# Kernel optimization log

Hardware: AMD Instinct MI355X
Metric: run time of the kernel (lower is better)

Reference implementation:

```python
import jax, jax.numpy as jnp
import numpy as np

N_NODES = 100000
N_EDGES = 640000
DIM = 128
N_LAYERS = 3


def setup_inputs() -> dict:
    key = jax.random.key(0)
    k1, k2, k3, k4, k5 = jax.random.split(key, 5)
    nodes = jax.random.normal(k1, (N_NODES, DIM), dtype=jnp.float32)
    edges = jax.random.randint(k2, (2, N_EDGES), 0, N_NODES, dtype=jnp.int64)
    # GCNConv weights: one [DIM, DIM] linear + bias per layer
    W = jax.random.normal(k3, (N_LAYERS, DIM, DIM), dtype=jnp.float32) * (1.0 / np.sqrt(DIM))
    b = jnp.zeros((N_LAYERS, DIM), dtype=jnp.float32)
    # classifier head Linear(DIM, 2)
    clf_W = jax.random.normal(k4, (DIM, 2), dtype=jnp.float32) * (1.0 / np.sqrt(DIM))
    clf_b = jnp.zeros((2,), dtype=jnp.float32)
    return {"nodes": nodes, "edges": edges, "W": W, "b": b, "clf_W": clf_W, "clf_b": clf_b}


def _gcn_layer(x, src, dst, dinv, W, b):
    # PyG GCNConv: x' = D^{-1/2} (A + I) D^{-1/2} (x W) + b
    x = x @ W                                      # [N, D]
    norm = dinv[src] * dinv[dst]                   # [E+N]
    msgs = x[src] * norm[:, None]                  # gather + scale, [E+N, D]
    return jax.ops.segment_sum(msgs, dst, num_segments=x.shape[0]) + b


def reference(nodes, edges, W, b, clf_W, clf_b):
    N = nodes.shape[0]
    loops = jnp.arange(N, dtype=edges.dtype)
    src = jnp.concatenate([edges[0], loops])       # add self-loops
    dst = jnp.concatenate([edges[1], loops])
    deg = jax.ops.segment_sum(jnp.ones_like(dst, dtype=nodes.dtype), dst, num_segments=N)
    dinv = jnp.where(deg > 0, jax.lax.rsqrt(deg), 0.0)
    x = nodes
    for i in range(W.shape[0]):
        x = jax.nn.relu(_gcn_layer(x, src, dst, dinv, W[i], b[i]))
    return x @ clf_W + clf_b                       # [N, 2]
```

## Files before the change

kernel.cpp:

```cpp
#include <hip/hip_runtime.h>
#include <hip/hip_bf16.h>

#define N_NODES 100000
#define N_EDGES 640000
#define DIM 128
#define NE_TOT (N_NODES + N_EDGES)

typedef unsigned short u16;
typedef unsigned int u32;
typedef __attribute__((ext_vector_type(8))) short bf16x8;
typedef __attribute__((ext_vector_type(4))) float f32x4;
typedef __attribute__((ext_vector_type(8))) unsigned short us8;

__device__ __forceinline__ u16 f2bf(float f) {
    u32 u = __float_as_uint(f);
    u32 r = (u + 0x7fffu + ((u >> 16) & 1u)) >> 16;
    return (u16)r;
}
__device__ __forceinline__ float bf2f(u16 h) { return __uint_as_float(((u32)h) << 16); }

__device__ __forceinline__ void gload16(const void* g, void* l) {
    __builtin_amdgcn_global_load_lds(
        (const __attribute__((address_space(1))) u32*)g,
        (__attribute__((address_space(3))) u32*)l, 16, 0, 0);
}


__global__ void init_deg_kernel(int* deg, int n) {
    int i = blockIdx.x * blockDim.x + threadIdx.x;
    if (i < n) deg[i] = 1;
}

__global__ void count_deg_kernel(const int* __restrict__ edges, int* deg, int e) {
    int i = blockIdx.x * blockDim.x + threadIdx.x;
    if (i < e) atomicAdd(&deg[edges[N_EDGES + i]], 1);
}

__global__ void scan1_kernel(const int* __restrict__ deg, int* off, int* bsums, int n) {
    __shared__ int lds[256];
    int t = threadIdx.x;
    int base = blockIdx.x * 1024 + t * 4;
    int v[4]; int s = 0;
#pragma unroll
    for (int j = 0; j < 4; j++) { int idx = base + j; v[j] = (idx < n) ? deg[idx] : 0; s += v[j]; }
    lds[t] = s; __syncthreads();
    for (int d = 1; d < 256; d <<= 1) {
        int x = 0;
        if (t >= d) x = lds[t - d];
        __syncthreads();
        if (t >= d) lds[t] += x;
        __syncthreads();
    }
    if (t == 255) bsums[blockIdx.x] = lds[255];
    int run = lds[t] - s;
#pragma unroll
    for (int j = 0; j < 4; j++) { int idx = base + j; if (idx < n) off[idx] = run; run += v[j]; }
}

__global__ void scan2_kernel(int* bsums, int nchunks) {
    __shared__ int lds[128];
    int t = threadIdx.x;
    int v = (t < nchunks) ? bsums[t] : 0;
    lds[t] = v; __syncthreads();
    for (int d = 1; d < 128; d <<= 1) {
        int x = 0;
        if (t >= d) x = lds[t - d];
        __syncthreads();
        if (t >= d) lds[t] += x;
        __syncthreads();
    }
    if (t < nchunks) bsums[t] = lds[t] - v;
}

__global__ void scan3_kernel(int* off, const int* __restrict__ bsums, const int* __restrict__ deg,
                             int* cursor, float* dinv, int n) {
    int i = blockIdx.x * blockDim.x + threadIdx.x;
    if (i < n) {
        int o = off[i] + bsums[i >> 10];
        off[i] = o;
        cursor[i] = o;
        dinv[i] = 1.0f / sqrtf((float)deg[i]);
    }
}

__global__ void fill_csr_kernel(const int* __restrict__ edges, int* cursor, int* csr) {
    int i = blockIdx.x * blockDim.x + threadIdx.x;
    if (i < N_NODES) {
        int p = atomicAdd(&cursor[i], 1);
        csr[p] = i;
    } else if (i < NE_TOT) {
        int e = i - N_NODES;
        int s = edges[e];
        int d = edges[N_EDGES + e];
        int p = atomicAdd(&cursor[d], 1);
        csr[p] = s;
    }
}

__global__ void wsplit_kernel(const float* __restrict__ W, u16* __restrict__ WhiT, u16* __restrict__ WloT) {
    int i = blockIdx.x * 256 + threadIdx.x;
    int l = i >> 14; int r = i & 16383; int k = r >> 7; int c = r & 127;
    float w = W[i];
    u16 h = f2bf(w);
    u16 lo = f2bf(w - bf2f(h));
    u32 inner = ((u32)(k * 2)) ^ (((u32)c & 7u) << 4);
    size_t db = (size_t)l * 32768 + (size_t)c * 256 + inner;
    *(u16*)((char*)WhiT + db) = h;
    *(u16*)((char*)WloT + db) = lo;
}

__global__ void aggregate_kernel(const float* __restrict__ x, u16* __restrict__ yhi, u16* __restrict__ ylo,
                                 const int* __restrict__ off, const int* __restrict__ csr,
                                 const float* __restrict__ dinv, int n) {
    int wid = (blockIdx.x * blockDim.x + threadIdx.x) >> 6;
    int lane = threadIdx.x & 63;
    if (wid >= n) return;
    int start = off[wid];
    int end = (wid == n - 1) ? NE_TOT : off[wid + 1];
    int d0 = lane * 2;
    float ax = 0.f, ay = 0.f;
    for (int k = start; k < end; k++) {
        int s = csr[k];
        float w = dinv[s];
        float2 xv = *reinterpret_cast<const float2*>(x + (size_t)s * DIM + d0);
        ax += xv.x * w;
        ay += xv.y * w;
    }
    float di = dinv[wid];
    float vx = ax * di, vy = ay * di;
    u16 hx = f2bf(vx); u16 lx = f2bf(vx - bf2f(hx));
    u16 hy = f2bf(vy); u16 ly = f2bf(vy - bf2f(hy));
    u32 inner = ((u32)(lane * 4)) ^ (((u32)wid & 7u) << 4);
    *(u32*)((char*)yhi + (size_t)wid * 256 + inner) = (u32)hx | ((u32)hy << 16);
    *(u32*)((char*)ylo + (size_t)wid * 256 + inner) = (u32)lx | ((u32)ly << 16);
}

__device__ __forceinline__ bf16x8 lds_frag(const char* base, int row, int kbyte) {
    int off = row * 256 + (kbyte ^ ((row & 7) << 4));
    return __builtin_bit_cast(bf16x8, *(const us8*)(base + off));
}

__global__ __launch_bounds__(512, 1) void gemm_mfma_kernel(
        const u16* __restrict__ Yhi, const u16* __restrict__ Ylo,
        const u16* __restrict__ WhiT, const u16* __restrict__ WloT,
        const float* __restrict__ bias, float* __restrict__ out, int M) {
    __shared__ char smem[131072];
    char* Ah = smem;
    char* Al = smem + 32768;
    char* Bh = smem + 65536;
    char* Bl = smem + 98304;
    const int t = threadIdx.x;
    const int lane = t & 63, w = t >> 6;
    const int rowbase = blockIdx.x * 128;

#pragma unroll
    for (int it = 0; it < 4; it++) {
        int p = w * 4096 + it * 1024 + lane * 16;
        int rl = p >> 8;
        int rg = rowbase + rl; rg = (rg < M) ? rg : (M - 1);
        int inner = p & 255;
        gload16((const char*)Yhi + (size_t)rg * 256 + inner, Ah + w * 4096 + it * 1024);
        gload16((const char*)Ylo + (size_t)rg * 256 + inner, Al + w * 4096 + it * 1024);
        gload16((const char*)WhiT + p, Bh + w * 4096 + it * 1024);
        gload16((const char*)WloT + p, Bl + w * 4096 + it * 1024);
    }
    __syncthreads();

    const int wr = w >> 1, wc = w & 1;
    const int lr = lane & 15, kh = lane >> 4;
    f32x4 acc[2][4] = {};

#pragma unroll
    for (int ks = 0; ks < 4; ks++) {
        int kb = ks * 64 + kh * 16;
        bf16x8 ah[2], al[2], bh[4], bl[4];
#pragma unroll
        for (int ri = 0; ri < 2; ri++) {
            ah[ri] = lds_frag(Ah, wr * 32 + ri * 16 + lr, kb);
            al[ri] = lds_frag(Al, wr * 32 + ri * 16 + lr, kb);
        }
#pragma unroll
        for (int ci = 0; ci < 4; ci++) {
            bh[ci] = lds_frag(Bh, wc * 64 + ci * 16 + lr, kb);
            bl[ci] = lds_frag(Bl, wc * 64 + ci * 16 + lr, kb);
        }
#pragma unroll
        for (int ri = 0; ri < 2; ri++)
#pragma unroll
            for (int ci = 0; ci < 4; ci++) {
                acc[ri][ci] = __builtin_amdgcn_mfma_f32_16x16x32_bf16(ah[ri], bh[ci], acc[ri][ci], 0, 0, 0);
                acc[ri][ci] = __builtin_amdgcn_mfma_f32_16x16x32_bf16(ah[ri], bl[ci], acc[ri][ci], 0, 0, 0);
                acc[ri][ci] = __builtin_amdgcn_mfma_f32_16x16x32_bf16(al[ri], bh[ci], acc[ri][ci], 0, 0, 0);
            }
    }

#pragma unroll
    for (int ri = 0; ri < 2; ri++)
#pragma unroll
        for (int ci = 0; ci < 4; ci++) {
            int col = wc * 64 + ci * 16 + lr;
            float bc = bias[col];
            int r0 = rowbase + wr * 32 + ri * 16 + kh * 4;
#pragma unroll
            for (int j = 0; j < 4; j++) {
                int r = r0 + j;
                if (r < M) out[(size_t)r * 128 + col] = fmaxf(acc[ri][ci][j] + bc, 0.f);
            }
        }
}

__global__ void classifier_kernel(const float* __restrict__ x, const float* __restrict__ clfW,
                                  const float* __restrict__ clfb, float* __restrict__ out, int n) {
    int wid = (blockIdx.x * blockDim.x + threadIdx.x) >> 6;
    int lane = threadIdx.x & 63;
    if (wid >= n) return;
    float w00 = clfW[2 * lane], w01 = clfW[2 * lane + 1];
    float w10 = clfW[2 * (lane + 64)], w11 = clfW[2 * (lane + 64) + 1];
    float x0 = x[(size_t)wid * DIM + lane];
    float x1 = x[(size_t)wid * DIM + lane + 64];
    float a0 = x0 * w00 + x1 * w10;
    float a1 = x0 * w01 + x1 * w11;
#pragma unroll
    for (int d = 32; d > 0; d >>= 1) {
        a0 += __shfl_down(a0, d);
        a1 += __shfl_down(a1, d);
    }
    if (lane == 0) {
        out[2 * wid]     = a0 + clfb[0];
        out[2 * wid + 1] = a1 + clfb[1];
    }
}

extern "C" void kernel_launch(void* const* d_in, const int* in_sizes, int n_in,
                              void* d_out, int out_size, void* d_ws, size_t ws_size,
                              hipStream_t stream) {
    const float* nodes = (const float*)d_in[0];
    const int*   edges = (const int*)d_in[1];
    const float* W     = (const float*)d_in[2];
    const float* b     = (const float*)d_in[3];
    const float* clfW  = (const float*)d_in[4];
    const float* clfb  = (const float*)d_in[5];
    float* out = (float*)d_out;

    const int N = N_NODES, E = N_EDGES;

    float* X    = (float*)d_ws;
    u16* Yhi    = (u16*)(X + (size_t)N * DIM);
    u16* Ylo    = Yhi + (size_t)N * DIM;
    u16* WhiT   = Ylo + (size_t)N * DIM;
    u16* WloT   = WhiT + 3 * DIM * DIM;
    float* dinv = (float*)(WloT + 3 * DIM * DIM);
    int* deg    = (int*)(dinv + N);
    int* off    = deg + N;
    int* cursor = off + N;
    int* csr    = cursor + N;
    int* bsums  = csr + NE_TOT;

    const int nchunks = (N + 1023) / 1024;

    wsplit_kernel<<<(3 * DIM * DIM) / 256, 256, 0, stream>>>(W, WhiT, WloT);
    init_deg_kernel<<<(N + 255) / 256, 256, 0, stream>>>(deg, N);
    count_deg_kernel<<<(E + 255) / 256, 256, 0, stream>>>(edges, deg, E);
    scan1_kernel<<<nchunks, 256, 0, stream>>>(deg, off, bsums, N);
    scan2_kernel<<<1, 128, 0, stream>>>(bsums, nchunks);
    scan3_kernel<<<(N + 255) / 256, 256, 0, stream>>>(off, bsums, deg, cursor, dinv, N);
    fill_csr_kernel<<<(NE_TOT + 255) / 256, 256, 0, stream>>>(edges, cursor, csr);

    const int aggBlocks = (N + 3) / 4;
    const int gemmBlocks = (N + 127) / 128;

    aggregate_kernel<<<aggBlocks, 256, 0, stream>>>(nodes, Yhi, Ylo, off, csr, dinv, N);
    gemm_mfma_kernel<<<gemmBlocks, 512, 0, stream>>>(Yhi, Ylo, WhiT, WloT, b, X, N);

    aggregate_kernel<<<aggBlocks, 256, 0, stream>>>(X, Yhi, Ylo, off, csr, dinv, N);
    gemm_mfma_kernel<<<gemmBlocks, 512, 0, stream>>>(Yhi, Ylo, WhiT + DIM * DIM, WloT + DIM * DIM,
                                                     b + DIM, X, N);

    aggregate_kernel<<<aggBlocks, 256, 0, stream>>>(X, Yhi, Ylo, off, csr, dinv, N);
    gemm_mfma_kernel<<<gemmBlocks, 512, 0, stream>>>(Yhi, Ylo, WhiT + 2 * DIM * DIM, WloT + 2 * DIM * DIM,
                                                     b + 2 * DIM, X, N);

    classifier_kernel<<<aggBlocks, 256, 0, stream>>>(X, clfW, clfb, out, N);
}
```

Baseline: 558.4 us.

## Aggregate four nodes per wavefront and read GEMM weights from global memory

The aggregation kernel now assigns 16 lanes per node (4 nodes per wave). Each lane loads two float4 vectors per edge and writes 16-byte bf16 hi/lo chunks, which raises memory-level parallelism and vector width for the gather. The GEMM drops the LDS staging of the split weights and reads weight fragments straight from global memory through lds_frag. This halves LDS use and allows more blocks per CU. It risks uncoalesced global weight reads in the inner MFMA loop, and lds_frag applied to a global pointer relies on generic addressing.

```diff
diff --git a/kernel.cpp b/kernel.cpp
--- a/kernel.cpp
+++ b/kernel.cpp
@@ -112,27 +112,40 @@
 __global__ void aggregate_kernel(const float* __restrict__ x, u16* __restrict__ yhi, u16* __restrict__ ylo,
                                  const int* __restrict__ off, const int* __restrict__ csr,
                                  const float* __restrict__ dinv, int n) {
-    int wid = (blockIdx.x * blockDim.x + threadIdx.x) >> 6;
+    int gw = (blockIdx.x * blockDim.x + threadIdx.x) >> 6;
     int lane = threadIdx.x & 63;
-    if (wid >= n) return;
-    int start = off[wid];
-    int end = (wid == n - 1) ? NE_TOT : off[wid + 1];
-    int d0 = lane * 2;
-    float ax = 0.f, ay = 0.f;
+    int grp = lane >> 4;
+    int l4  = lane & 15;
+    int node = gw * 4 + grp;
+    if (node >= n) return;
+    int start = off[node];
+    int end = (node == n - 1) ? NE_TOT : off[node + 1];
+    float a[8] = {0.f, 0.f, 0.f, 0.f, 0.f, 0.f, 0.f, 0.f};
     for (int k = start; k < end; k++) {
         int s = csr[k];
         float w = dinv[s];
-        float2 xv = *reinterpret_cast<const float2*>(x + (size_t)s * DIM + d0);
-        ax += xv.x * w;
-        ay += xv.y * w;
-    }
-    float di = dinv[wid];
-    float vx = ax * di, vy = ay * di;
-    u16 hx = f2bf(vx); u16 lx = f2bf(vx - bf2f(hx));
-    u16 hy = f2bf(vy); u16 ly = f2bf(vy - bf2f(hy));
-    u32 inner = ((u32)(lane * 4)) ^ (((u32)wid & 7u) << 4);
-    *(u32*)((char*)yhi + (size_t)wid * 256 + inner) = (u32)hx | ((u32)hy << 16);
-    *(u32*)((char*)ylo + (size_t)wid * 256 + inner) = (u32)lx | ((u32)ly << 16);
+        const float* row = x + (size_t)s * DIM + l4 * 8;
+        float4 v0 = *reinterpret_cast<const float4*>(row);
+        float4 v1 = *reinterpret_cast<const float4*>(row + 4);
+        a[0] += v0.x * w; a[1] += v0.y * w; a[2] += v0.z * w; a[3] += v0.w * w;
+        a[4] += v1.x * w; a[5] += v1.y * w; a[6] += v1.z * w; a[7] += v1.w * w;
+    }
+    float di = dinv[node];
+    u16 h[8], lo[8];
+#pragma unroll
+    for (int j = 0; j < 8; j++) {
+        float v = a[j] * di;
+        h[j]  = f2bf(v);
+        lo[j] = f2bf(v - bf2f(h[j]));
+    }
+    u32 inner = ((u32)(l4 * 16)) ^ (((u32)node & 7u) << 4);
+    uint4 hv, lv;
+    hv.x = (u32)h[0]  | ((u32)h[1]  << 16); hv.y = (u32)h[2]  | ((u32)h[3]  << 16);
+    hv.z = (u32)h[4]  | ((u32)h[5]  << 16); hv.w = (u32)h[6]  | ((u32)h[7]  << 16);
+    lv.x = (u32)lo[0] | ((u32)lo[1] << 16); lv.y = (u32)lo[2] | ((u32)lo[3] << 16);
+    lv.z = (u32)lo[4] | ((u32)lo[5] << 16); lv.w = (u32)lo[6] | ((u32)lo[7] << 16);
+    *reinterpret_cast<uint4*>((char*)yhi + (size_t)node * 256 + inner) = hv;
+    *reinterpret_cast<uint4*>((char*)ylo + (size_t)node * 256 + inner) = lv;
 }
 
 __device__ __forceinline__ bf16x8 lds_frag(const char* base, int row, int kbyte) {
@@ -140,15 +153,13 @@
     return __builtin_bit_cast(bf16x8, *(const us8*)(base + off));
 }
 
-__global__ __launch_bounds__(512, 1) void gemm_mfma_kernel(
+__global__ __launch_bounds__(512, 4) void gemm_mfma_kernel(
         const u16* __restrict__ Yhi, const u16* __restrict__ Ylo,
         const u16* __restrict__ WhiT, const u16* __restrict__ WloT,
         const float* __restrict__ bias, float* __restrict__ out, int M) {
-    __shared__ char smem[131072];
+    __shared__ char smem[65536];
     char* Ah = smem;
     char* Al = smem + 32768;
-    char* Bh = smem + 65536;
-    char* Bl = smem + 98304;
     const int t = threadIdx.x;
     const int lane = t & 63, w = t >> 6;
     const int rowbase = blockIdx.x * 128;
@@ -161,8 +172,6 @@
         int inner = p & 255;
         gload16((const char*)Yhi + (size_t)rg * 256 + inner, Ah + w * 4096 + it * 1024);
         gload16((const char*)Ylo + (size_t)rg * 256 + inner, Al + w * 4096 + it * 1024);
-        gload16((const char*)WhiT + p, Bh + w * 4096 + it * 1024);
-        gload16((const char*)WloT + p, Bl + w * 4096 + it * 1024);
     }
     __syncthreads();
 
@@ -181,8 +190,9 @@
         }
 #pragma unroll
         for (int ci = 0; ci < 4; ci++) {
-            bh[ci] = lds_frag(Bh, wc * 64 + ci * 16 + lr, kb);
-            bl[ci] = lds_frag(Bl, wc * 64 + ci * 16 + lr, kb);
+            int brow = wc * 64 + ci * 16 + lr;
+            bh[ci] = lds_frag((const char*)WhiT, brow, kb);
+            bl[ci] = lds_frag((const char*)WloT, brow, kb);
         }
 #pragma unroll
         for (int ri = 0; ri < 2; ri++)
@@ -266,7 +276,7 @@
     scan3_kernel<<<(N + 255) / 256, 256, 0, stream>>>(off, bsums, deg, cursor, dinv, N);
     fill_csr_kernel<<<(NE_TOT + 255) / 256, 256, 0, stream>>>(edges, cursor, csr);
 
-    const int aggBlocks = (N + 3) / 4;
+    const int aggBlocks = (N + 15) / 16;
     const int gemmBlocks = (N + 127) / 128;
 
     aggregate_kernel<<<aggBlocks, 256, 0, stream>>>(nodes, Yhi, Ylo, off, csr, dinv, N);
@@ -280,5 +290,5 @@
     gemm_mfma_kernel<<<gemmBlocks, 512, 0, stream>>>(Yhi, Ylo, WhiT + 2 * DIM * DIM, WloT + 2 * DIM * DIM,
                                                      b + 2 * DIM, X, N);
 
-    classifier_kernel<<<aggBlocks, 256, 0, stream>>>(X, clfW, clfb, out, N);
-}
+    classifier_kernel<<<(N + 3) / 4, 256, 0, stream>>>(X, clfW, clfb, out, N);
+}
```

New measurement: 453.2 us. 1.23x faster.
